# Optimization experiments

Measured on AMD Instinct MI355X. Metric: run time of the kernel, lower is better.

Reference implementation:

```python
import jax, jax.numpy as jnp
import numpy as np

D_MODEL = 512
N_HEADS = 8
D_HEAD = D_MODEL // N_HEADS  # 64
D_PROJ = 32
H_ENC = 512
D_MAX = 32


def _rope_cache(T, d):
    pos = jnp.arange(T, dtype=jnp.float32)[:, None]                      # [T,1]
    freqs = 1.0 / (10000.0 ** (jnp.arange(0, d, 2, dtype=jnp.float32) / d))  # [d/2]
    ang = pos * freqs                                                     # [T,d/2]
    return jnp.cos(ang), jnp.sin(ang)


def _apply_rope(x, cos, sin):
    # x: [B,H,T,D]
    T = x.shape[2]
    d2 = x.shape[-1] // 2
    x1, x2 = x[..., :d2], x[..., d2:]
    c = cos[:T][None, None]
    s = sin[:T][None, None]
    return jnp.concatenate([x1 * c - x2 * s, x2 * c + x1 * s], axis=-1)


def _layernorm(a, g, b, eps=1e-5):
    m = jnp.mean(a, axis=-1, keepdims=True)
    v = jnp.mean((a - m) ** 2, axis=-1, keepdims=True)
    return (a - m) * jax.lax.rsqrt(v + eps) * g + b


def setup_inputs() -> dict:
    key = jax.random.key(0)
    ks = jax.random.split(key, 8)
    B, T = 2, 2048
    x = jax.random.normal(ks[0], (B, T, D_MODEL), jnp.float32)
    q_projs = jax.random.normal(ks[1], (N_HEADS, D_MODEL, D_PROJ), jnp.float32) * D_MODEL ** -0.5
    k_projs = jax.random.normal(ks[2], (N_HEADS, D_MODEL, D_PROJ), jnp.float32) * D_MODEL ** -0.5
    w_v = jax.random.normal(ks[3], (D_MODEL, D_MODEL), jnp.float32) * D_MODEL ** -0.5
    w_proj = jax.random.normal(ks[4], (D_MODEL, D_MODEL), jnp.float32) * 0.02
    q_gain = jnp.ones((N_HEADS,), jnp.float32)
    enc_w0 = jax.random.normal(ks[5], (H_ENC, D_MODEL), jnp.float32) * D_MODEL ** -0.5
    enc_ln1_g = jnp.ones((H_ENC,), jnp.float32)
    enc_ln1_b = jnp.zeros((H_ENC,), jnp.float32)
    enc_w1 = jax.random.normal(ks[6], (H_ENC, H_ENC), jnp.float32) * H_ENC ** -0.5
    enc_ln2_g = jnp.ones((H_ENC,), jnp.float32)
    enc_ln2_b = jnp.zeros((H_ENC,), jnp.float32)
    enc_w2 = jax.random.normal(ks[7], (H_ENC, H_ENC), jnp.float32) * H_ENC ** -0.5
    enc_w_out = jax.random.normal(jax.random.fold_in(key, 99), (D_MAX, H_ENC), jnp.float32) * H_ENC ** -0.5
    coord_temp = jnp.ones((D_MAX,), jnp.float32)
    return {"x": x, "q_projs": q_projs, "k_projs": k_projs, "w_v": w_v, "w_proj": w_proj,
            "q_gain": q_gain, "enc_w0": enc_w0, "enc_ln1_g": enc_ln1_g, "enc_ln1_b": enc_ln1_b,
            "enc_w1": enc_w1, "enc_ln2_g": enc_ln2_g, "enc_ln2_b": enc_ln2_b, "enc_w2": enc_w2,
            "enc_w_out": enc_w_out, "coord_temp": coord_temp}


def reference(x, q_projs, k_projs, w_v, w_proj, q_gain,
              enc_w0, enc_ln1_g, enc_ln1_b, enc_w1, enc_ln2_g, enc_ln2_b,
              enc_w2, enc_w_out, coord_temp):
    B, T, C = x.shape
    # ---- CausalSelfAttention (qk_mode='per_head_proj') ----
    q = jnp.einsum('btd,hdo->bhto', x, q_projs)                    # [B,H,T,Dp]
    k = jnp.einsum('btd,hdo->bhto', x, k_projs)                    # [B,H,T,Dp]
    v = (x @ w_v.T).reshape(B, T, N_HEADS, D_HEAD).transpose(0, 2, 1, 3)  # [B,H,T,Dh]
    cos, sin = _rope_cache(T, D_PROJ)
    q = _apply_rope(q, cos, sin)
    k = _apply_rope(k, cos, sin)
    q = q * q_gain[None, :, None, None]
    scale = 1.0 / jnp.sqrt(jnp.asarray(D_PROJ, q.dtype))
    scores = jnp.einsum('bhto,bhso->bhts', q, k) * scale           # [B,H,T,T]
    causal = jnp.tril(jnp.ones((T, T), bool))
    scores = jnp.where(causal, scores, jnp.asarray(-1e30, scores.dtype))
    attn = jax.nn.softmax(scores, axis=-1)
    y = jnp.einsum('bhts,bhsd->bhtd', attn, v)                     # [B,H,T,Dh]
    # self-alignment subtraction (F.normalize eps = 1e-12)
    v_norm = v / jnp.maximum(jnp.linalg.norm(v, axis=-1, keepdims=True), 1e-12)
    self_align = jnp.sum(y * v_norm, axis=-1, keepdims=True) * v_norm
    y = y - self_align
    y = y.transpose(0, 2, 1, 3).reshape(B, T, C)
    h = x + y @ w_proj.T                                           # residual
    # ---- ChartEncoder (d_in == H so proj0 is Identity) ----
    he = h @ enc_w0.T
    he = h + jax.nn.silu(_layernorm(he, enc_ln1_g, enc_ln1_b) @ enc_w1.T)
    he = he + jax.nn.silu(_layernorm(he, enc_ln2_g, enc_ln2_b) @ enc_w2.T)
    h_rms = he * jax.lax.rsqrt(jnp.mean(he * he, axis=-1, keepdims=True) + 1e-6)
    z_raw = h_rms @ enc_w_out.T                                    # [B,T,d_max]
    z = jnp.tanh(z_raw / (jax.nn.softplus(coord_temp) + 1e-4))
    return z
```

## Files before the change

kernel.cpp:

```cpp
#include <hip/hip_runtime.h>
#include <math.h>

typedef unsigned short u16;
typedef __attribute__((ext_vector_type(8))) short short8;
typedef __attribute__((ext_vector_type(4))) float floatx4;

__device__ __forceinline__ float b2f(u16 u) { return __uint_as_float(((unsigned)u) << 16); }
__device__ __forceinline__ u16 f2b(float f) {
  unsigned u = __float_as_uint(f);
  return (u16)((u + 0x7fffu + ((u >> 16) & 1u)) >> 16);
}

__global__ __launch_bounds__(256) void prep_cast(const float* __restrict__ x, const float* __restrict__ wpr,
                                                 const float* __restrict__ w0, const float* __restrict__ w1,
                                                 const float* __restrict__ w2, const float* __restrict__ qp,
                                                 const float* __restrict__ kp, const float* __restrict__ wv,
                                                 u16* __restrict__ XB, u16* __restrict__ WPRb,
                                                 u16* __restrict__ W0b, u16* __restrict__ W1b,
                                                 u16* __restrict__ W2b, u16* __restrict__ wcat) {
  int bi = blockIdx.x, tid = threadIdx.x;
  if (bi < 2048) {
    int i = bi * 256 + tid;
    float4 v = ((const float4*)x)[i];
    ushort4 o; o.x = f2b(v.x); o.y = f2b(v.y); o.z = f2b(v.z); o.w = f2b(v.w);
    ((ushort4*)XB)[i] = o;
  } else if (bi < 3072) {
    int i = (bi - 2048) * 256 + tid;
    int sel = i >> 16, j = i & 65535;
    const float* s = sel == 0 ? wpr : sel == 1 ? w0 : sel == 2 ? w1 : w2;
    float4 v = ((const float4*)s)[j];
    ushort4 o; o.x = f2b(v.x); o.y = f2b(v.y); o.z = f2b(v.z); o.w = f2b(v.w);
    if (sel == 0) {
      ((ushort4*)WPRb)[j] = o;
    } else {
      u16* d = sel == 1 ? W0b : sel == 2 ? W1b : W2b;
      int n = j >> 7, k4 = (j & 127) << 2;
      int lane = (((k4 >> 3) & 3) << 4) | (n & 15);
      int dst = (((n >> 4) * 16 + (k4 >> 5)) << 9) + lane * 8 + (k4 & 7);
      *(ushort4*)(d + dst) = o;
    }
  } else {
    int i = (bi - 3072) * 256 + tid;
    int d = i & 511, c = i >> 9;
    float v;
    if (c < 512) {
      int hh = c >> 5, o = c & 31;
      const float* src = (hh < 8) ? qp : kp;
      int h = hh & 7;
      v = src[(h * 512 + d) * 32 + o];
    } else {
      v = wv[(c - 512) * 512 + d];
    }
    wcat[i] = f2b(v);
  }
}

template <int EPI, bool DUAL>
__global__ __launch_bounds__(256) void mgemm(const u16* __restrict__ A, const u16* __restrict__ Bw,
                                             const float* __restrict__ X, float* __restrict__ C,
                                             u16* __restrict__ Cb, int N) {
  __shared__ u16 As[64][72];
  __shared__ u16 Bs[64][72];
  const int tid = threadIdx.x;
  const int bm = blockIdx.y, bn = blockIdx.x;
  const int lane = tid & 63, wave = tid >> 6;
  const int wm = wave >> 1, wn = wave & 1;
  const int quad = lane >> 4, l16 = lane & 15;
  const int sr = tid >> 2;
  const int sk = (tid & 3) << 4;
  floatx4 acc[2][2] = {};
  const u16* Ap = A + (size_t)(bm * 64 + sr) * 512 + sk;
  const u16* Bp = Bw + (size_t)(bn * 64 + sr) * 512 + sk;
  uint4 a0 = *(const uint4*)(Ap);
  uint4 a1 = *(const uint4*)(Ap + 8);
  uint4 b0 = *(const uint4*)(Bp);
  uint4 b1 = *(const uint4*)(Bp + 8);
  for (int k0 = 0; k0 < 512; k0 += 64) {
    __syncthreads();
    *(uint4*)&As[sr][sk] = a0;
    *(uint4*)&As[sr][sk + 8] = a1;
    *(uint4*)&Bs[sr][sk] = b0;
    *(uint4*)&Bs[sr][sk + 8] = b1;
    __syncthreads();
    if (k0 + 64 < 512) {
      a0 = *(const uint4*)(Ap + k0 + 64);
      a1 = *(const uint4*)(Ap + k0 + 72);
      b0 = *(const uint4*)(Bp + k0 + 64);
      b1 = *(const uint4*)(Bp + k0 + 72);
    }
#pragma unroll
    for (int kk = 0; kk < 2; kk++) {
      short8 af0 = *(const short8*)&As[wm * 32 + l16][kk * 32 + quad * 8];
      short8 af1 = *(const short8*)&As[wm * 32 + 16 + l16][kk * 32 + quad * 8];
      short8 bf0 = *(const short8*)&Bs[wn * 32 + l16][kk * 32 + quad * 8];
      short8 bf1 = *(const short8*)&Bs[wn * 32 + 16 + l16][kk * 32 + quad * 8];
      acc[0][0] = __builtin_amdgcn_mfma_f32_16x16x32_bf16(af0, bf0, acc[0][0], 0, 0, 0);
      acc[0][1] = __builtin_amdgcn_mfma_f32_16x16x32_bf16(af0, bf1, acc[0][1], 0, 0, 0);
      acc[1][0] = __builtin_amdgcn_mfma_f32_16x16x32_bf16(af1, bf0, acc[1][0], 0, 0, 0);
      acc[1][1] = __builtin_amdgcn_mfma_f32_16x16x32_bf16(af1, bf1, acc[1][1], 0, 0, 0);
    }
  }
#pragma unroll
  for (int mt = 0; mt < 2; mt++)
#pragma unroll
    for (int r = 0; r < 4; r++) {
      int row = bm * 64 + wm * 32 + mt * 16 + quad * 4 + r;
#pragma unroll
      for (int nt = 0; nt < 2; nt++) {
        int col = bn * 64 + wn * 32 + nt * 16 + l16;
        float v = acc[mt][nt][r];
        if (EPI == 1) {
          v += X[(size_t)row * 512 + col];
        } else if (EPI == 2) {
          float xv = X[(size_t)row * 512 + col];
          v = xv + v / (1.f + __expf(-v));
        }
        C[(size_t)row * N + col] = v;
        if (DUAL) Cb[(size_t)row * N + col] = f2b(v);
      }
    }
}

__global__ __launch_bounds__(256) void qkv_gemm(const u16* __restrict__ A, const u16* __restrict__ Bw,
                                                const float* __restrict__ qgain,
                                                u16* __restrict__ Qb, u16* __restrict__ Kb,
                                                u16* __restrict__ Vt, float* __restrict__ Vf) {
  __shared__ u16 As[64][72];
  __shared__ u16 Bs[64][72];
  const int tid = threadIdx.x;
  const int bm = blockIdx.y, bn = blockIdx.x;
  const int lane = tid & 63, wave = tid >> 6;
  const int wm = wave >> 1, wn = wave & 1;
  const int quad = lane >> 4, l16 = lane & 15;
  const int sr = tid >> 2;
  const int sk = (tid & 3) << 4;
  floatx4 acc[2][2] = {};
  const u16* Ap = A + (size_t)(bm * 64 + sr) * 512 + sk;
  const u16* Bp = Bw + (size_t)(bn * 64 + sr) * 512 + sk;
  uint4 a0 = *(const uint4*)(Ap);
  uint4 a1 = *(const uint4*)(Ap + 8);
  uint4 b0 = *(const uint4*)(Bp);
  uint4 b1 = *(const uint4*)(Bp + 8);
  for (int k0 = 0; k0 < 512; k0 += 64) {
    __syncthreads();
    *(uint4*)&As[sr][sk] = a0;
    *(uint4*)&As[sr][sk + 8] = a1;
    *(uint4*)&Bs[sr][sk] = b0;
    *(uint4*)&Bs[sr][sk + 8] = b1;
    __syncthreads();
    if (k0 + 64 < 512) {
      a0 = *(const uint4*)(Ap + k0 + 64);
      a1 = *(const uint4*)(Ap + k0 + 72);
      b0 = *(const uint4*)(Bp + k0 + 64);
      b1 = *(const uint4*)(Bp + k0 + 72);
    }
#pragma unroll
    for (int kk = 0; kk < 2; kk++) {
      short8 af0 = *(const short8*)&As[wm * 32 + l16][kk * 32 + quad * 8];
      short8 af1 = *(const short8*)&As[wm * 32 + 16 + l16][kk * 32 + quad * 8];
      short8 bf0 = *(const short8*)&Bs[wn * 32 + l16][kk * 32 + quad * 8];
      short8 bf1 = *(const short8*)&Bs[wn * 32 + 16 + l16][kk * 32 + quad * 8];
      acc[0][0] = __builtin_amdgcn_mfma_f32_16x16x32_bf16(af0, bf0, acc[0][0], 0, 0, 0);
      acc[0][1] = __builtin_amdgcn_mfma_f32_16x16x32_bf16(af0, bf1, acc[0][1], 0, 0, 0);
      acc[1][0] = __builtin_amdgcn_mfma_f32_16x16x32_bf16(af1, bf0, acc[1][0], 0, 0, 0);
      acc[1][1] = __builtin_amdgcn_mfma_f32_16x16x32_bf16(af1, bf1, acc[1][1], 0, 0, 0);
    }
  }
  if (bn < 8) {
    const bool isq = (bn < 4);
    const int h = (isq ? bn : bn - 4) * 2 + wn;
    const float gq = isq ? qgain[h] * (0.17677669529663687f * 1.4426950408889634f) : 1.f;
    const float freq = powf(10000.f, -(float)l16 / 16.f);
    u16* outb = (isq ? Qb : Kb);
#pragma unroll
    for (int mt = 0; mt < 2; mt++)
#pragma unroll
      for (int r = 0; r < 4; r++) {
        int row = bm * 64 + wm * 32 + mt * 16 + quad * 4 + r;
        int t = row & 2047, b = row >> 11;
        float s, c;
        sincosf((float)t * freq, &s, &c);
        float q0 = acc[mt][0][r], q1 = acc[mt][1][r];
        u16* base = outb + ((size_t)((b * 8 + h) * 2048 + t)) * 32;
        if (isq) {
          base[l16] = f2b((q0 * c - q1 * s) * gq);
          base[l16 + 16] = f2b((q1 * c + q0 * s) * gq);
        } else {
          base[l16] = f2b(q0 * c - q1 * s);
          base[l16 + 16] = f2b(q1 * c + q0 * s);
        }
      }
  } else {
    const int h = bn - 8;
    const int b = bm >> 5;
#pragma unroll
    for (int mt = 0; mt < 2; mt++)
#pragma unroll
      for (int r = 0; r < 4; r++) {
        int row = bm * 64 + wm * 32 + mt * 16 + quad * 4 + r;
#pragma unroll
        for (int nt = 0; nt < 2; nt++) {
          int d = wn * 32 + nt * 16 + l16;
          Vf[(size_t)row * 512 + h * 64 + d] = acc[mt][nt][r];
        }
      }
    __syncthreads();
#pragma unroll
    for (int mt = 0; mt < 2; mt++)
#pragma unroll
      for (int r = 0; r < 4; r++) {
        int rl = wm * 32 + mt * 16 + quad * 4 + r;
#pragma unroll
        for (int nt = 0; nt < 2; nt++) {
          int d = wn * 32 + nt * 16 + l16;
          As[d][rl] = f2b(acc[mt][nt][r]);
        }
      }
    __syncthreads();
    const int bh = b * 8 + h;
    const int t0 = (bm & 31) * 64;
    const int dim = tid >> 2, ch = (tid & 3) << 4;
    u16* dst = Vt + ((size_t)(bh * 64 + dim)) * 2048 + t0 + ch;
    *(uint4*)dst = *(const uint4*)&As[dim][ch];
    *(uint4*)(dst + 8) = *(const uint4*)&As[dim][ch + 8];
  }
}

__global__ __launch_bounds__(256) void attn_split(const u16* __restrict__ Qb, const u16* __restrict__ Kb,
                                                  const u16* __restrict__ Vt, float* __restrict__ PO,
                                                  float* __restrict__ PL) {
  const int bi = blockIdx.x;
  const int bh = bi & 15;
  const int q0i = (bi >> 4) & 15;
  const int rem = bi >> 8;
  const int qt = (rem & 1) ? (31 - q0i) : q0i;
  const int s = rem >> 1;
  const int tid = threadIdx.x;
  const int w = tid >> 6, lane = tid & 63, quad = lane >> 4, l16 = lane & 15;
  __shared__ u16 Vts[64][72];
  __shared__ u16 Ps[4][16][72];

  const int mid = (qt + 1) >> 1;
  const int kt_beg = s ? mid : 0;
  const int kt_end = s ? (qt + 1) : mid;

  short8 qfrag = *(const short8*)(Qb + ((size_t)(bh * 2048 + qt * 64 + w * 16 + l16)) * 32 + quad * 8);
  floatx4 o_acc[4] = {};
  float l_part[4] = {0.f, 0.f, 0.f, 0.f};
  const u16* Kbase = Kb + (size_t)bh * 2048 * 32;
  const u16* Vtb = Vt + (size_t)bh * 64 * 2048;
  const int vr = tid >> 2, vc = (tid & 3) << 4;

  uint4 v0 = {}, v1 = {};
  short8 kf[4] = {};
  if (kt_beg < kt_end) {
    const u16* src = Vtb + (size_t)vr * 2048 + kt_beg * 64 + vc;
    v0 = *(const uint4*)src;
    v1 = *(const uint4*)(src + 8);
#pragma unroll
    for (int nt = 0; nt < 4; nt++)
      kf[nt] = *(const short8*)(Kbase + (size_t)(kt_beg * 64 + nt * 16 + l16) * 32 + quad * 8);
  }

  for (int kt = kt_beg; kt < kt_end; ++kt) {
    __syncthreads();
    *(uint4*)&Vts[vr][vc] = v0;
    *(uint4*)&Vts[vr][vc + 8] = v1;
    __syncthreads();
    const bool more = (kt + 1 < kt_end);
    uint4 v0n = {}, v1n = {};
    short8 kfn[4] = {};
    if (more) {
      const u16* src = Vtb + (size_t)vr * 2048 + (kt + 1) * 64 + vc;
      v0n = *(const uint4*)src;
      v1n = *(const uint4*)(src + 8);
#pragma unroll
      for (int nt = 0; nt < 4; nt++)
        kfn[nt] = *(const short8*)(Kbase + (size_t)((kt + 1) * 64 + nt * 16 + l16) * 32 + quad * 8);
    }

    floatx4 s_acc[4];
    __builtin_amdgcn_s_setprio(1);
#pragma unroll
    for (int nt = 0; nt < 4; nt++) {
      floatx4 zz = {0.f, 0.f, 0.f, 0.f};
      s_acc[nt] = __builtin_amdgcn_mfma_f32_16x16x32_bf16(qfrag, kf[nt], zz, 0, 0, 0);
    }
    __builtin_amdgcn_s_setprio(0);
    const bool diag = (kt == qt);
#pragma unroll
    for (int r = 0; r < 4; r++) {
      int mloc = w * 16 + quad * 4 + r;
      float psum = 0.f;
#pragma unroll
      for (int nt = 0; nt < 4; nt++) {
        float p = __builtin_amdgcn_exp2f(s_acc[nt][r]);
        if (diag && (nt * 16 + l16) > mloc) p = 0.f;
        psum += p;
        Ps[w][quad * 4 + r][nt * 16 + l16] = f2b(p);
      }
      l_part[r] += psum;
    }
    __builtin_amdgcn_s_setprio(1);
#pragma unroll
    for (int kc = 0; kc < 2; kc++) {
      short8 pf = *(const short8*)&Ps[w][l16][kc * 32 + quad * 8];
#pragma unroll
      for (int nt = 0; nt < 4; nt++) {
        short8 vf = *(const short8*)&Vts[nt * 16 + l16][kc * 32 + quad * 8];
        o_acc[nt] = __builtin_amdgcn_mfma_f32_16x16x32_bf16(pf, vf, o_acc[nt], 0, 0, 0);
      }
    }
    __builtin_amdgcn_s_setprio(0);
    v0 = v0n; v1 = v1n;
#pragma unroll
    for (int nt = 0; nt < 4; nt++) kf[nt] = kfn[nt];
  }

  const int pidx = (bh * 32 + qt) * 2 + s;
  float* pob = PO + (size_t)pidx * 4096;
#pragma unroll
  for (int r = 0; r < 4; r++) {
    float ls = l_part[r];
#pragma unroll
    for (int mk = 1; mk < 16; mk <<= 1) ls += __shfl_xor(ls, mk, 64);
    int row = w * 16 + quad * 4 + r;
#pragma unroll
    for (int nt = 0; nt < 4; nt++) pob[row * 64 + nt * 16 + l16] = o_acc[nt][r];
    if (l16 == 0) PL[pidx * 64 + row] = ls;
  }
}

__global__ __launch_bounds__(256) void attn_combine(const float* __restrict__ PO, const float* __restrict__ PL,
                                                    const float* __restrict__ Vf, u16* __restrict__ y2b) {
  int ridx = blockIdx.x * 4 + (threadIdx.x >> 6);
  int lane = threadIdx.x & 63;
  int bh = ridx >> 11, tok = ridx & 2047;
  int qt = tok >> 6, row = tok & 63;
  int pidx = (bh * 32 + qt) * 2;
  const float* p0 = PO + (size_t)pidx * 4096 + row * 64;
  float o = p0[lane] + p0[4096 + lane];
  float l = PL[pidx * 64 + row] + PL[(pidx + 1) * 64 + row];
  float yv = o / l;
  int b = bh >> 3, h = bh & 7;
  float vv = Vf[(size_t)(b * 2048 + tok) * 512 + h * 64 + lane];
  float ss = vv * vv, dot = yv * vv;
#pragma unroll
  for (int mk = 1; mk < 64; mk <<= 1) {
    ss += __shfl_xor(ss, mk, 64);
    dot += __shfl_xor(dot, mk, 64);
  }
  float coef = dot / fmaxf(ss, 1e-24f);
  y2b[(size_t)(b * 2048 + tok) * 512 + h * 64 + lane] = f2b(yv - coef * vv);
}

#define HPAD 516

__device__ __forceinline__ int enc_swz(int row, int col) {
  return row * 512 + ((((col >> 3) ^ (row & 7)) << 3) | (col & 7));
}

__device__ __forceinline__ void enc_gemm(const u16* __restrict__ inb, const u16* __restrict__ Wf,
                                         floatx4* acc, int wave, int l16, int quad, int lane, int krot) {
  const u16* wb = Wf + ((size_t)(wave * 4 * 16) << 9) + lane * 8;
  short8 aB[4];
  short8 bB[4][4];
#pragma unroll
  for (int p = 0; p < 4; p++) {
    const int kc = (p + krot) & 15;
    aB[p] = *(const short8*)(inb + enc_swz(l16, kc * 32 + quad * 8));
#pragma unroll
    for (int nt = 0; nt < 4; nt++)
      bB[p][nt] = *(const short8*)(wb + (((nt * 16) + kc) << 9));
  }
#pragma unroll
  for (int ks = 0; ks < 16; ks++) {
    const int cur = ks & 3;
#pragma unroll
    for (int nt = 0; nt < 4; nt++)
      acc[nt] = __builtin_amdgcn_mfma_f32_16x16x32_bf16(aB[cur], bB[cur][nt], acc[nt], 0, 0, 0);
    if (ks + 4 < 16) {
      const int kn = (ks + 4 + krot) & 15;
      aB[cur] = *(const short8*)(inb + enc_swz(l16, kn * 32 + quad * 8));
#pragma unroll
      for (int nt = 0; nt < 4; nt++)
        bB[cur][nt] = *(const short8*)(wb + (((nt * 16) + kn) << 9));
    }
  }
}

__global__ __launch_bounds__(512) void enc_fused(const float* __restrict__ H, const u16* __restrict__ W0b,
                                                 const u16* __restrict__ W1b, const u16* __restrict__ W2b,
                                                 const float* __restrict__ g1v, const float* __restrict__ b1v,
                                                 const float* __restrict__ g2v, const float* __restrict__ b2v,
                                                 const float* __restrict__ wout, const float* __restrict__ ct,
                                                 float* __restrict__ z) {
  __shared__ u16 curb[16 * 512];
  __shared__ u16 lnb[16 * 512];
  __shared__ float hres[16][HPAD];
  __shared__ float red[8][16][2];

  const int tid = threadIdx.x;
  const int wave = tid >> 6, lane = tid & 63, quad = lane >> 4, l16 = lane & 15;
  const int row0 = blockIdx.x * 16;
  const int n0 = wave * 64;
  const int krot = (blockIdx.x >> 3) & 15;

#pragma unroll
  for (int j = 0; j < 4; j++) {
    int idx = j * 512 + tid;
    int row = idx >> 7, c4 = idx & 127;
    float4 v = ((const float4*)H)[(size_t)(row0 + row) * 128 + c4];
    *(float4*)&hres[row][c4 * 4] = v;
    int col = c4 * 4;
    curb[enc_swz(row, col + 0)] = f2b(v.x);
    curb[enc_swz(row, col + 1)] = f2b(v.y);
    curb[enc_swz(row, col + 2)] = f2b(v.z);
    curb[enc_swz(row, col + 3)] = f2b(v.w);
  }
  __syncthreads();

  floatx4 acc1[4] = {};
  enc_gemm(curb, W0b, acc1, wave, l16, quad, lane, krot);

  {
#pragma unroll
    for (int r = 0; r < 4; r++) {
      float s = 0.f, q = 0.f;
#pragma unroll
      for (int nt = 0; nt < 4; nt++) { float v = acc1[nt][r]; s += v; q = fmaf(v, v, q); }
#pragma unroll
      for (int mk = 1; mk < 16; mk <<= 1) { s += __shfl_xor(s, mk, 64); q += __shfl_xor(q, mk, 64); }
      if (l16 == 0) { red[wave][quad * 4 + r][0] = s; red[wave][quad * 4 + r][1] = q; }
    }
    __syncthreads();
#pragma unroll
    for (int r = 0; r < 4; r++) {
      int R = quad * 4 + r;
      float st = 0.f, qt2 = 0.f;
#pragma unroll
      for (int w2 = 0; w2 < 8; w2++) { st += red[w2][R][0]; qt2 += red[w2][R][1]; }
      float mean = st * (1.f / 512.f);
      float inv = rsqrtf(qt2 * (1.f / 512.f) - mean * mean + 1e-5f);
#pragma unroll
      for (int nt = 0; nt < 4; nt++) {
        int col = n0 + nt * 16 + l16;
        lnb[enc_swz(R, col)] = f2b((acc1[nt][r] - mean) * inv * g1v[col] + b1v[col]);
      }
    }
    __syncthreads();
  }

  floatx4 acc2[4] = {};
  enc_gemm(lnb, W1b, acc2, wave, l16, quad, lane, krot);
  float hval[4][4];
  {
#pragma unroll
    for (int r = 0; r < 4; r++) {
      int R = quad * 4 + r;
      float s = 0.f, q = 0.f;
#pragma unroll
      for (int nt = 0; nt < 4; nt++) {
        int col = n0 + nt * 16 + l16;
        float u = acc2[nt][r];
        float hv = hres[R][col] + u / (1.f + __expf(-u));
        hres[R][col] = hv;
        hval[nt][r] = hv;
        s += hv; q = fmaf(hv, hv, q);
      }
#pragma unroll
      for (int mk = 1; mk < 16; mk <<= 1) { s += __shfl_xor(s, mk, 64); q += __shfl_xor(q, mk, 64); }
      if (l16 == 0) { red[wave][R][0] = s; red[wave][R][1] = q; }
    }
    __syncthreads();
#pragma unroll
    for (int r = 0; r < 4; r++) {
      int R = quad * 4 + r;
      float st = 0.f, qt2 = 0.f;
#pragma unroll
      for (int w2 = 0; w2 < 8; w2++) { st += red[w2][R][0]; qt2 += red[w2][R][1]; }
      float mean = st * (1.f / 512.f);
      float inv = rsqrtf(qt2 * (1.f / 512.f) - mean * mean + 1e-5f);
#pragma unroll
      for (int nt = 0; nt < 4; nt++) {
        int col = n0 + nt * 16 + l16;
        lnb[enc_swz(R, col)] = f2b((hval[nt][r] - mean) * inv * g2v[col] + b2v[col]);
      }
    }
    __syncthreads();
  }

  floatx4 acc3[4] = {};
  enc_gemm(lnb, W2b, acc3, wave, l16, quad, lane, krot);
  {
#pragma unroll
    for (int r = 0; r < 4; r++) {
      int R = quad * 4 + r;
      float q = 0.f;
#pragma unroll
      for (int nt = 0; nt < 4; nt++) {
        int col = n0 + nt * 16 + l16;
        float u = acc3[nt][r];
        float hv = hres[R][col] + u / (1.f + __expf(-u));
        hres[R][col] = hv;
        q = fmaf(hv, hv, q);
      }
#pragma unroll
      for (int mk = 1; mk < 16; mk <<= 1) q += __shfl_xor(q, mk, 64);
      if (l16 == 0) red[wave][R][1] = q;
    }
    __syncthreads();
  }

  {
    const int n = lane & 31, kh = lane >> 5;
    float rinv[2], pacc[2] = {0.f, 0.f};
#pragma unroll
    for (int rr = 0; rr < 2; rr++) {
      int R = wave * 2 + rr;
      float qt2 = 0.f;
#pragma unroll
      for (int w2 = 0; w2 < 8; w2++) qt2 += red[w2][R][1];
      rinv[rr] = rsqrtf(qt2 * (1.f / 512.f) + 1e-6f);
    }
    for (int kc = 0; kc < 64; kc++) {
      int k = kh * 256 + kc * 4;
      float4 wv = *(const float4*)(wout + (size_t)n * 512 + k);
#pragma unroll
      for (int rr = 0; rr < 2; rr++) {
        float4 hv = *(const float4*)&hres[wave * 2 + rr][k];
        pacc[rr] = fmaf(wv.x, hv.x, fmaf(wv.y, hv.y, fmaf(wv.z, hv.z, fmaf(wv.w, hv.w, pacc[rr]))));
      }
    }
#pragma unroll
    for (int rr = 0; rr < 2; rr++) pacc[rr] += __shfl_xor(pacc[rr], 32, 64);
    if (kh == 0) {
      float c = ct[n];
      float sp = (c > 20.f) ? c : log1pf(__expf(c));
#pragma unroll
      for (int rr = 0; rr < 2; rr++)
        z[(size_t)(row0 + wave * 2 + rr) * 32 + n] = tanhf(pacc[rr] * rinv[rr] / (sp + 1e-4f));
    }
  }
}

extern "C" void kernel_launch(void* const* d_in, const int* in_sizes, int n_in,
                              void* d_out, int out_size, void* d_ws, size_t ws_size,
                              hipStream_t stream) {
  const float* x = (const float*)d_in[0];
  const float* qp = (const float*)d_in[1];
  const float* kp = (const float*)d_in[2];
  const float* wv = (const float*)d_in[3];
  const float* wpr = (const float*)d_in[4];
  const float* qg = (const float*)d_in[5];
  const float* w0 = (const float*)d_in[6];
  const float* g1 = (const float*)d_in[7];
  const float* b1 = (const float*)d_in[8];
  const float* w1 = (const float*)d_in[9];
  const float* g2 = (const float*)d_in[10];
  const float* b2 = (const float*)d_in[11];
  const float* w2 = (const float*)d_in[12];
  const float* wout = (const float*)d_in[13];
  const float* ct = (const float*)d_in[14];
  float* z = (float*)d_out;

  float* ws = (float*)d_ws;
  const size_t MEG = 1024 * 1024;
  float* A_V = ws;
  u16* A_Qb = (u16*)(ws + 4 * MEG);
  u16* A_Kb = (u16*)(ws + 4 * MEG + 524288);
  u16* A_Vt = (u16*)(ws + 5 * MEG);
  float* A_PO = ws + 6 * MEG;
  u16* A_Y2b = (u16*)(ws + 10 * MEG);
  float* A_H = ws + 11 * MEG;
  u16* XB = (u16*)(ws + 13 * MEG);
  float* A_PL = ws + 13 * MEG;
  u16* WCATb = (u16*)(ws + 14 * MEG);
  u16* WPRb = WCATb + 524288;
  u16* W0b = WPRb + 262144;
  u16* W1b = W0b + 262144;
  u16* W2b = W1b + 262144;

  hipLaunchKernelGGL(prep_cast, dim3(5120), dim3(256), 0, stream, x, wpr, w0, w1, w2, qp, kp, wv,
                     XB, WPRb, W0b, W1b, W2b, WCATb);
  hipLaunchKernelGGL(qkv_gemm, dim3(16, 64), dim3(256), 0, stream, XB, WCATb, qg,
                     A_Qb, A_Kb, A_Vt, A_V);
  hipLaunchKernelGGL(attn_split, dim3(1024), dim3(256), 0, stream, A_Qb, A_Kb, A_Vt, A_PO, A_PL);
  hipLaunchKernelGGL(attn_combine, dim3(8192), dim3(256), 0, stream, A_PO, A_PL, A_V, A_Y2b);
  hipLaunchKernelGGL((mgemm<1, false>), dim3(8, 64), dim3(256), 0, stream, A_Y2b, WPRb, x, A_H,
                     (u16*)nullptr, 512);
  hipLaunchKernelGGL(enc_fused, dim3(256), dim3(512), 0, stream, A_H, W0b, W1b, W2b,
                     g1, b1, g2, b2, wout, ct, z);
}
```

Baseline: 181.0 us.

## Fuse split-K attention and combine into one kernel with inline self-alignment

Removes the two-way key split in attention and the separate combine kernel. Each block now walks the full causal key range for its query tile and applies the normalization and self-alignment subtraction in registers before writing bf16 output. This drops the fp32 partial-output round trip through global memory and one launch. In exchange the grid halves to 512 blocks with longer, more unbalanced causal loops, which reduces parallelism on a GPU with many CUs.

```diff
diff --git a/kernel.cpp b/kernel.cpp
--- a/kernel.cpp
+++ b/kernel.cpp
@@ -226,23 +226,18 @@
   }
 }
 
-__global__ __launch_bounds__(256) void attn_split(const u16* __restrict__ Qb, const u16* __restrict__ Kb,
-                                                  const u16* __restrict__ Vt, float* __restrict__ PO,
-                                                  float* __restrict__ PL) {
+__global__ __launch_bounds__(256) void attn_fused(const u16* __restrict__ Qb, const u16* __restrict__ Kb,
+                                                  const u16* __restrict__ Vt, const float* __restrict__ Vf,
+                                                  u16* __restrict__ y2b) {
   const int bi = blockIdx.x;
   const int bh = bi & 15;
   const int q0i = (bi >> 4) & 15;
-  const int rem = bi >> 8;
-  const int qt = (rem & 1) ? (31 - q0i) : q0i;
-  const int s = rem >> 1;
+  const int hi = bi >> 8;
+  const int qt = hi ? (31 - q0i) : q0i;
   const int tid = threadIdx.x;
   const int w = tid >> 6, lane = tid & 63, quad = lane >> 4, l16 = lane & 15;
   __shared__ u16 Vts[64][72];
   __shared__ u16 Ps[4][16][72];
-
-  const int mid = (qt + 1) >> 1;
-  const int kt_beg = s ? mid : 0;
-  const int kt_end = s ? (qt + 1) : mid;
 
   short8 qfrag = *(const short8*)(Qb + ((size_t)(bh * 2048 + qt * 64 + w * 16 + l16)) * 32 + quad * 8);
   floatx4 o_acc[4] = {};
@@ -251,23 +246,23 @@
   const u16* Vtb = Vt + (size_t)bh * 64 * 2048;
   const int vr = tid >> 2, vc = (tid & 3) << 4;
 
-  uint4 v0 = {}, v1 = {};
-  short8 kf[4] = {};
-  if (kt_beg < kt_end) {
-    const u16* src = Vtb + (size_t)vr * 2048 + kt_beg * 64 + vc;
+  uint4 v0, v1;
+  short8 kf[4];
+  {
+    const u16* src = Vtb + (size_t)vr * 2048 + vc;
     v0 = *(const uint4*)src;
     v1 = *(const uint4*)(src + 8);
 #pragma unroll
     for (int nt = 0; nt < 4; nt++)
-      kf[nt] = *(const short8*)(Kbase + (size_t)(kt_beg * 64 + nt * 16 + l16) * 32 + quad * 8);
-  }
-
-  for (int kt = kt_beg; kt < kt_end; ++kt) {
+      kf[nt] = *(const short8*)(Kbase + (size_t)(nt * 16 + l16) * 32 + quad * 8);
+  }
+
+  for (int kt = 0; kt <= qt; ++kt) {
     __syncthreads();
     *(uint4*)&Vts[vr][vc] = v0;
     *(uint4*)&Vts[vr][vc + 8] = v1;
     __syncthreads();
-    const bool more = (kt + 1 < kt_end);
+    const bool more = (kt < qt);
     uint4 v0n = {}, v1n = {};
     short8 kfn[4] = {};
     if (more) {
@@ -317,41 +312,34 @@
     for (int nt = 0; nt < 4; nt++) kf[nt] = kfn[nt];
   }
 
-  const int pidx = (bh * 32 + qt) * 2 + s;
-  float* pob = PO + (size_t)pidx * 4096;
+  const int b = bh >> 3, h = bh & 7;
 #pragma unroll
   for (int r = 0; r < 4; r++) {
     float ls = l_part[r];
 #pragma unroll
     for (int mk = 1; mk < 16; mk <<= 1) ls += __shfl_xor(ls, mk, 64);
-    int row = w * 16 + quad * 4 + r;
-#pragma unroll
-    for (int nt = 0; nt < 4; nt++) pob[row * 64 + nt * 16 + l16] = o_acc[nt][r];
-    if (l16 == 0) PL[pidx * 64 + row] = ls;
-  }
-}
-
-__global__ __launch_bounds__(256) void attn_combine(const float* __restrict__ PO, const float* __restrict__ PL,
-                                                    const float* __restrict__ Vf, u16* __restrict__ y2b) {
-  int ridx = blockIdx.x * 4 + (threadIdx.x >> 6);
-  int lane = threadIdx.x & 63;
-  int bh = ridx >> 11, tok = ridx & 2047;
-  int qt = tok >> 6, row = tok & 63;
-  int pidx = (bh * 32 + qt) * 2;
-  const float* p0 = PO + (size_t)pidx * 4096 + row * 64;
-  float o = p0[lane] + p0[4096 + lane];
-  float l = PL[pidx * 64 + row] + PL[(pidx + 1) * 64 + row];
-  float yv = o / l;
-  int b = bh >> 3, h = bh & 7;
-  float vv = Vf[(size_t)(b * 2048 + tok) * 512 + h * 64 + lane];
-  float ss = vv * vv, dot = yv * vv;
-#pragma unroll
-  for (int mk = 1; mk < 64; mk <<= 1) {
-    ss += __shfl_xor(ss, mk, 64);
-    dot += __shfl_xor(dot, mk, 64);
-  }
-  float coef = dot / fmaxf(ss, 1e-24f);
-  y2b[(size_t)(b * 2048 + tok) * 512 + h * 64 + lane] = f2b(yv - coef * vv);
+    int tok = qt * 64 + w * 16 + quad * 4 + r;
+    float linv = 1.f / ls;
+    const float* vp = Vf + (size_t)(b * 2048 + tok) * 512 + h * 64 + l16;
+    float yv[4], vv[4];
+    float dot = 0.f, ss = 0.f;
+#pragma unroll
+    for (int nt = 0; nt < 4; nt++) {
+      yv[nt] = o_acc[nt][r] * linv;
+      vv[nt] = vp[nt * 16];
+      dot = fmaf(yv[nt], vv[nt], dot);
+      ss = fmaf(vv[nt], vv[nt], ss);
+    }
+#pragma unroll
+    for (int mk = 1; mk < 16; mk <<= 1) {
+      dot += __shfl_xor(dot, mk, 64);
+      ss += __shfl_xor(ss, mk, 64);
+    }
+    float coef = dot / fmaxf(ss, 1e-24f);
+    u16* op = y2b + (size_t)(b * 2048 + tok) * 512 + h * 64 + l16;
+#pragma unroll
+    for (int nt = 0; nt < 4; nt++) op[nt * 16] = f2b(yv[nt] - coef * vv[nt]);
+  }
 }
 
 #define HPAD 516
@@ -570,11 +558,9 @@
   u16* A_Qb = (u16*)(ws + 4 * MEG);
   u16* A_Kb = (u16*)(ws + 4 * MEG + 524288);
   u16* A_Vt = (u16*)(ws + 5 * MEG);
-  float* A_PO = ws + 6 * MEG;
   u16* A_Y2b = (u16*)(ws + 10 * MEG);
   float* A_H = ws + 11 * MEG;
   u16* XB = (u16*)(ws + 13 * MEG);
-  float* A_PL = ws + 13 * MEG;
   u16* WCATb = (u16*)(ws + 14 * MEG);
   u16* WPRb = WCATb + 524288;
   u16* W0b = WPRb + 262144;
@@ -585,8 +571,7 @@
                      XB, WPRb, W0b, W1b, W2b, WCATb);
   hipLaunchKernelGGL(qkv_gemm, dim3(16, 64), dim3(256), 0, stream, XB, WCATb, qg,
                      A_Qb, A_Kb, A_Vt, A_V);
-  hipLaunchKernelGGL(attn_split, dim3(1024), dim3(256), 0, stream, A_Qb, A_Kb, A_Vt, A_PO, A_PL);
-  hipLaunchKernelGGL(attn_combine, dim3(8192), dim3(256), 0, stream, A_PO, A_PL, A_V, A_Y2b);
+  hipLaunchKernelGGL(attn_fused, dim3(512), dim3(256), 0, stream, A_Qb, A_Kb, A_Vt, A_V, A_Y2b);
   hipLaunchKernelGGL((mgemm<1, false>), dim3(8, 64), dim3(256), 0, stream, A_Y2b, WPRb, x, A_H,
                      (u16*)nullptr, 512);
   hipLaunchKernelGGL(enc_fused, dim3(256), dim3(512), 0, stream, A_H, W0b, W1b, W2b,
```

New measurement: 174.8 us (median of 2 runs). 1.04x faster.
